# Optimization experiments

Hardware: AMD Instinct MI355X
Metric: run time of the kernel (lower is better)

The kernel has to match this reference:

```python
import jax, jax.numpy as jnp
import numpy as np

B, C, IN, H = 64, 128, 1024, 512  # batch, channels, input features (=='seq_length' arg), hidden


def setup_inputs() -> dict:
    key = jax.random.key(0)
    ks = jax.random.split(key, 9)
    s = 1.0 / np.sqrt(H)  # PyTorch LSTM init: U(-1/sqrt(H), 1/sqrt(H))
    u = lambda k, shape: jax.random.uniform(k, shape, jnp.float32, -s, s)
    return {
        "x": jax.random.normal(ks[0], (B, C, IN), jnp.float32),
        # layer 0: one weight set per direction (fwd, bwd)
        "W_ih0": u(ks[1], (2, 4 * H, IN)),
        "W_hh0": u(ks[2], (2, 4 * H, H)),
        "b_ih0": u(ks[3], (2, 4 * H)),
        "b_hh0": u(ks[4], (2, 4 * H)),
        # layers 1..2: input is concat of both directions (2H)
        "W_ih12": u(ks[5], (2, 2, 4 * H, 2 * H)),
        "W_hh12": u(ks[6], (2, 2, 4 * H, H)),
        "b_ih12": u(ks[7], (2, 2, 4 * H)),
        "b_hh12": u(ks[8], (2, 2, 4 * H)),
    }


def _cell(inp, W_ih, b_ih, b_hh):
    # One LSTM step from zero state (h0 = c0 = 0): W_hh @ h0 == 0, f*c0 == 0.
    gates = inp @ W_ih.T + b_ih + b_hh  # [N, 4H]
    i, f, g, o = jnp.split(gates, 4, axis=-1)  # PyTorch gate order: i, f, g, o
    c = jax.nn.sigmoid(i) * jnp.tanh(g)
    return jax.nn.sigmoid(o) * jnp.tanh(c)  # h, shape [N, H]


def reference(x, W_ih0, W_hh0, b_ih0, b_hh0, W_ih12, W_hh12, b_ih12, b_hh12):
    b, c, n = x.shape
    # Each channel is an independent seq-len-1 LSTM call with zero init state,
    # so fold channels into the batch dimension. W_hh* contribute nothing (h0=0).
    xb = x.reshape(b * c, n)
    h = jnp.concatenate(
        [_cell(xb, W_ih0[d], b_ih0[d], b_hh0[d]) for d in range(2)], axis=-1
    )  # [b*c, 2H]
    for l in range(2):  # layers 1 and 2
        h = jnp.concatenate(
            [_cell(h, W_ih12[l, d], b_ih12[l, d], b_hh12[l, d]) for d in range(2)],
            axis=-1,
        )
    return h.reshape(b, c, 2 * H)  # [batch, channels, 2*hidden]
```

## Files before the change

### kernel.cpp

```cpp
#include <hip/hip_runtime.h>


typedef float f32x4 __attribute__((ext_vector_type(4)));
typedef short short8 __attribute__((ext_vector_type(8)));
typedef unsigned short u16;

#define NP 3072
#define MROWS 8192
#define KDIM 1024
#define BM 256
#define BN 384
#define BK 32
#define LDS_TILE 40960

__device__ __forceinline__ u16 f2bf(float f) {
  unsigned u = __float_as_uint(f);
  u += 0x7fffu + ((u >> 16) & 1u);
  return (u16)(u >> 16);
}
__device__ __forceinline__ float sigmoid_f(float x) {
  return 1.0f / (1.0f + __expf(-x));
}
__device__ __forceinline__ float tanh_f(float x) {
  float xc = fminf(fmaxf(x, -15.0f), 15.0f);
  float e = __expf(2.0f * xc);
  return (e - 1.0f) / (e + 1.0f);
}
__device__ __forceinline__ void gload_lds16(const void* g, void* l) {
  __builtin_amdgcn_global_load_lds((const __attribute__((address_space(1))) void*)g,
                                   (__attribute__((address_space(3))) void*)l,
                                   16, 0, 0);
}


__global__ __launch_bounds__(256) void k_convert_x(const float* __restrict__ x,
                                                   u16* __restrict__ out) {
  int tid = blockIdx.x * 256 + threadIdx.x;
  const float4* src = (const float4*)x + (size_t)tid * 2;
  float4 v0 = src[0], v1 = src[1];
  union { u16 u[8]; uint4 v; } r;
  r.u[0] = f2bf(v0.x); r.u[1] = f2bf(v0.y); r.u[2] = f2bf(v0.z); r.u[3] = f2bf(v0.w);
  r.u[4] = f2bf(v1.x); r.u[5] = f2bf(v1.y); r.u[6] = f2bf(v1.z); r.u[7] = f2bf(v1.w);
  ((uint4*)out)[tid] = r.v;
}

__global__ __launch_bounds__(256) void k_pack_w(const float* __restrict__ Wih0,
                                                const float* __restrict__ Wih12,
                                                u16* __restrict__ P) {
  int tid = blockIdx.x * 256 + threadIdx.x;
  int s   = tid / (NP * 128);
  int rem = tid - s * (NP * 128);
  int p   = rem >> 7;
  int k8  = rem & 127;
  int hb = p / 48;
  int pr = p - hb * 48;
  int gs = pr >> 4;
  int hl = pr & 15;
  int hcol = hb * 16 + hl;
  int dir = hcol >> 9;
  int h   = hcol & 511;
  int og  = (gs == 0) ? 0 : (gs + 1);
  const float* src;
  if (s == 0)
    src = Wih0 + ((size_t)(dir * 2048 + og * 512 + h)) * 1024 + k8 * 8;
  else
    src = Wih12 + ((size_t)(((s - 1) * 2 + dir) * 2048 + og * 512 + h)) * 1024 + k8 * 8;
  float4 v0 = ((const float4*)src)[0];
  float4 v1 = ((const float4*)src)[1];
  union { u16 u[8]; uint4 v; } r;
  r.u[0] = f2bf(v0.x); r.u[1] = f2bf(v0.y); r.u[2] = f2bf(v0.z); r.u[3] = f2bf(v0.w);
  r.u[4] = f2bf(v1.x); r.u[5] = f2bf(v1.y); r.u[6] = f2bf(v1.z); r.u[7] = f2bf(v1.w);
  ((uint4*)P)[tid] = r.v;
}

__global__ __launch_bounds__(256) void k_pack_bias(const float* __restrict__ bih0,
                                                   const float* __restrict__ bhh0,
                                                   const float* __restrict__ bih12,
                                                   const float* __restrict__ bhh12,
                                                   float* __restrict__ pb) {
  int tid = blockIdx.x * 256 + threadIdx.x;
  if (tid >= 3 * NP) return;
  int s = tid / NP;
  int p = tid - s * NP;
  int hb = p / 48;
  int pr = p - hb * 48;
  int gs = pr >> 4;
  int hl = pr & 15;
  int hcol = hb * 16 + hl;
  int dir = hcol >> 9;
  int h   = hcol & 511;
  int og  = (gs == 0) ? 0 : (gs + 1);
  int j   = og * 512 + h;
  float v;
  if (s == 0) {
    int i = dir * 2048 + j;
    v = bih0[i] + bhh0[i];
  } else {
    int i = ((s - 1) * 2 + dir) * 2048 + j;
    v = bih12[i] + bhh12[i];
  }
  pb[tid] = v;
}


#define BAR()    __builtin_amdgcn_s_barrier()
#define SCHEDB() __builtin_amdgcn_sched_barrier(0)
#define WAITV(N) asm volatile("s_waitcnt vmcnt(" #N ")" ::: "memory")
#define MM(Macc, Aop, Bop) Macc = __builtin_amdgcn_mfma_f32_16x16x32_bf16(Aop, Bop, Macc, 0, 0, 0)

#define STAGE(BUF, KT) \
  { char* dst = lds + (BUF) * LDS_TILE + t * 16; \
    gload_lds16(srcA + (size_t)(KT) * BK,               dst); \
    gload_lds16(srcA + 128 * KDIM + (size_t)(KT) * BK,  dst + 8192); \
    gload_lds16(srcB + (size_t)(KT) * BK,               dst + 16384); \
    gload_lds16(srcB + 128 * KDIM + (size_t)(KT) * BK,  dst + 24576); \
    gload_lds16(srcB + 256 * KDIM + (size_t)(KT) * BK,  dst + 32768); }

#define KSTEP(RBUF, SBUF, KT, DOST, LASTT) \
  { \
    if (DOST) { STAGE(SBUF, (KT) + 2); } \
    const char* base = lds + (RBUF) * LDS_TILE; \
    short8 a0 = *(const short8*)(base + aBase); \
    short8 a1 = *(const short8*)(base + aBase + 1024); \
    short8 a2 = *(const short8*)(base + aBase + 2048); \
    short8 a3 = *(const short8*)(base + aBase + 3072); \
    short8 a4 = *(const short8*)(base + aBase + 4096); \
    short8 a5 = *(const short8*)(base + aBase + 5120); \
    short8 a6 = *(const short8*)(base + aBase + 6144); \
    short8 a7 = *(const short8*)(base + aBase + 7168); \
    short8 b0 = *(const short8*)(base + bBase); \
    short8 b1 = *(const short8*)(base + bBase + 1024); \
    short8 b2 = *(const short8*)(base + bBase + 2048); \
    __builtin_amdgcn_s_setprio(1); \
    MM(acc[0][0], a0, b0); MM(acc[1][0], a1, b0); MM(acc[2][0], a2, b0); MM(acc[3][0], a3, b0); \
    MM(acc[4][0], a4, b0); MM(acc[5][0], a5, b0); MM(acc[6][0], a6, b0); MM(acc[7][0], a7, b0); \
    MM(acc[0][1], a0, b1); MM(acc[1][1], a1, b1); MM(acc[2][1], a2, b1); MM(acc[3][1], a3, b1); \
    MM(acc[4][1], a4, b1); MM(acc[5][1], a5, b1); MM(acc[6][1], a6, b1); MM(acc[7][1], a7, b1); \
    MM(acc[0][2], a0, b2); MM(acc[1][2], a1, b2); MM(acc[2][2], a2, b2); MM(acc[3][2], a3, b2); \
    MM(acc[4][2], a4, b2); MM(acc[5][2], a5, b2); MM(acc[6][2], a6, b2); MM(acc[7][2], a7, b2); \
    __builtin_amdgcn_s_setprio(0); \
    b0 = *(const short8*)(base + bBase + 3072); \
    b1 = *(const short8*)(base + bBase + 4096); \
    b2 = *(const short8*)(base + bBase + 5120); \
    __builtin_amdgcn_s_setprio(1); \
    MM(acc[0][3], a0, b0); MM(acc[1][3], a1, b0); MM(acc[2][3], a2, b0); MM(acc[3][3], a3, b0); \
    MM(acc[4][3], a4, b0); MM(acc[5][3], a5, b0); MM(acc[6][3], a6, b0); MM(acc[7][3], a7, b0); \
    MM(acc[0][4], a0, b1); MM(acc[1][4], a1, b1); MM(acc[2][4], a2, b1); MM(acc[3][4], a3, b1); \
    MM(acc[4][4], a4, b1); MM(acc[5][4], a5, b1); MM(acc[6][4], a6, b1); MM(acc[7][4], a7, b1); \
    MM(acc[0][5], a0, b2); MM(acc[1][5], a1, b2); MM(acc[2][5], a2, b2); MM(acc[3][5], a3, b2); \
    MM(acc[4][5], a4, b2); MM(acc[5][5], a5, b2); MM(acc[6][5], a6, b2); MM(acc[7][5], a7, b2); \
    __builtin_amdgcn_s_setprio(0); \
    if (DOST) { WAITV(5); } \
    else if (!(LASTT)) { WAITV(0); } \
    if (!(LASTT)) { BAR(); SCHEDB(); } \
  }

template <bool F32OUT>
__global__ __launch_bounds__(512, 2) void k_lstm_gemmW(const u16* __restrict__ A,
                                                       const u16* __restrict__ Bp,
                                                       const float* __restrict__ bias,
                                                       void* __restrict__ outp) {
  __shared__ __align__(16) char lds[3 * LDS_TILE];
  const int t    = threadIdx.x;
  const int lane = t & 63;
  const int w    = t >> 6;
  const int wr   = w >> 2;
  const int wc   = w & 3;
  const int r16  = lane & 15, kg = lane >> 4;

  const int n_hw = blockIdx.y * gridDim.x + blockIdx.x;
  const int c    = n_hw & 7;
  const int wlc  = n_hw >> 3;
  const int bx   = (c & 1) * 4 + (wlc & 3);
  const int by   = (c >> 1) * 8 + (wlc >> 2);
  const int brow = by * BM;
  const int bn0  = bx * BN;

  const int slot = (kg ^ ((r16 >> 1) & 3)) << 4;
  const int aBase = wr * 8192 + r16 * 64 + slot;
  const int bBase = 16384 + wc * 6144 + r16 * 64 + slot;

  const int srow = t >> 2;
  const int koct = ((t & 3) ^ ((t >> 3) & 3)) << 3;
  const u16* srcA = A  + (size_t)(brow + srow) * KDIM + koct;
  const u16* srcB = Bp + (size_t)(bn0  + srow) * KDIM + koct;

  f32x4 acc[8][6];
#pragma unroll
  for (int m = 0; m < 8; ++m)
#pragma unroll
    for (int n = 0; n < 6; ++n) acc[m][n] = (f32x4){0.f, 0.f, 0.f, 0.f};

  STAGE(0, 0);
  STAGE(1, 1);
  WAITV(5);
  BAR(); SCHEDB();

  for (int k3 = 0; k3 < 10; ++k3) {
    int kt = k3 * 3;
    KSTEP(0, 2, kt + 0, 1, 0);
    KSTEP(1, 0, kt + 1, 1, 0);
    KSTEP(2, 1, kt + 2, 1, 0);
  }
  KSTEP(0, 0, 30, 0, 0);
  KSTEP(1, 0, 31, 0, 1);

#pragma unroll
  for (int trio = 0; trio < 2; ++trio) {
    int pbase = bn0 + wc * 96 + trio * 48;
    float biV = bias[pbase + r16];
    float bgV = bias[pbase + 16 + r16];
    float boV = bias[pbase + 32 + r16];
    int hcol = (bx * 8 + wc * 2 + trio) * 16 + r16;
#pragma unroll
    for (int m = 0; m < 8; ++m) {
      int rowb = brow + wr * 128 + m * 16 + kg * 4;
#pragma unroll
      for (int r = 0; r < 4; ++r) {
        float vi = acc[m][trio * 3 + 0][r] + biV;
        float vg = acc[m][trio * 3 + 1][r] + bgV;
        float vo = acc[m][trio * 3 + 2][r] + boV;
        float c2 = sigmoid_f(vi) * tanh_f(vg);
        float hv = sigmoid_f(vo) * tanh_f(c2);
        size_t oidx = (size_t)(rowb + r) * 1024 + hcol;
        if (F32OUT) ((float*)outp)[oidx] = hv;
        else        ((u16*)outp)[oidx]   = f2bf(hv);
      }
    }
  }
}

extern "C" void kernel_launch(void* const* d_in, const int* in_sizes, int n_in,
                              void* d_out, int out_size, void* d_ws, size_t ws_size,
                              hipStream_t stream) {
  const float* x     = (const float*)d_in[0];
  const float* Wih0  = (const float*)d_in[1];
  const float* bih0  = (const float*)d_in[3];
  const float* bhh0  = (const float*)d_in[4];
  const float* Wih12 = (const float*)d_in[5];
  const float* bih12 = (const float*)d_in[7];
  const float* bhh12 = (const float*)d_in[8];

  char* ws = (char*)d_ws;
  u16*   xbf = (u16*)ws;
  u16*   h1  = (u16*)(ws + 16777216);
  u16*   h2  = (u16*)(ws + 33554432);
  u16*   P3  = (u16*)(ws + 50331648);
  float* pb3 = (float*)(ws + 69206016);

  k_convert_x<<<4096, 256, 0, stream>>>(x, xbf);
  k_pack_w<<<4608, 256, 0, stream>>>(Wih0, Wih12, P3);
  k_pack_bias<<<36, 256, 0, stream>>>(bih0, bhh0, bih12, bhh12, pb3);

  dim3 grid(NP / BN, MROWS / BM);
  k_lstm_gemmW<false><<<grid, 512, 0, stream>>>(xbf, P3, pb3, h1);
  k_lstm_gemmW<false><<<grid, 512, 0, stream>>>(h1, P3 + (size_t)NP * KDIM, pb3 + NP, h2);
  k_lstm_gemmW<true ><<<grid, 512, 0, stream>>>(h2, P3 + (size_t)2 * NP * KDIM, pb3 + 2 * NP, d_out);
}
```

Measured before the change: 198.0 us.

## Halve GEMM tile width to 256x192 with 4 waves and double buffering

```diff
diff --git a/kernel.cpp b/kernel.cpp
--- a/kernel.cpp
+++ b/kernel.cpp
@@ -9,9 +9,9 @@
 #define MROWS 8192
 #define KDIM 1024
 #define BM 256
-#define BN 384
+#define BN 192
 #define BK 32
-#define LDS_TILE 40960
+#define LDS_TILE 28672
 
 __device__ __forceinline__ u16 f2bf(float f) {
   unsigned u = __float_as_uint(f);
@@ -111,68 +111,68 @@
 #define STAGE(BUF, KT) \
   { char* dst = lds + (BUF) * LDS_TILE + t * 16; \
     gload_lds16(srcA + (size_t)(KT) * BK,               dst); \
+    gload_lds16(srcA + 64 * KDIM + (size_t)(KT) * BK,   dst + 4096); \
     gload_lds16(srcA + 128 * KDIM + (size_t)(KT) * BK,  dst + 8192); \
+    gload_lds16(srcA + 192 * KDIM + (size_t)(KT) * BK,  dst + 12288); \
     gload_lds16(srcB + (size_t)(KT) * BK,               dst + 16384); \
-    gload_lds16(srcB + 128 * KDIM + (size_t)(KT) * BK,  dst + 24576); \
-    gload_lds16(srcB + 256 * KDIM + (size_t)(KT) * BK,  dst + 32768); }
-
-#define KSTEP(RBUF, SBUF, KT, DOST, LASTT) \
+    gload_lds16(srcB + 64 * KDIM + (size_t)(KT) * BK,   dst + 20480); \
+    gload_lds16(srcB + 128 * KDIM + (size_t)(KT) * BK,  dst + 24576); }
+
+#define KSTEP(RBUF, KT, DOST, LASTT) \
   { \
-    if (DOST) { STAGE(SBUF, (KT) + 2); } \
+    if (DOST) { STAGE((RBUF)^1, (KT)+1); } \
     const char* base = lds + (RBUF) * LDS_TILE; \
     short8 a0 = *(const short8*)(base + aBase); \
     short8 a1 = *(const short8*)(base + aBase + 1024); \
     short8 a2 = *(const short8*)(base + aBase + 2048); \
     short8 a3 = *(const short8*)(base + aBase + 3072); \
-    short8 a4 = *(const short8*)(base + aBase + 4096); \
-    short8 a5 = *(const short8*)(base + aBase + 5120); \
-    short8 a6 = *(const short8*)(base + aBase + 6144); \
-    short8 a7 = *(const short8*)(base + aBase + 7168); \
     short8 b0 = *(const short8*)(base + bBase); \
     short8 b1 = *(const short8*)(base + bBase + 1024); \
     short8 b2 = *(const short8*)(base + bBase + 2048); \
+    short8 b3 = *(const short8*)(base + bBase + 3072); \
+    short8 b4 = *(const short8*)(base + bBase + 4096); \
+    short8 b5 = *(const short8*)(base + bBase + 5120); \
     __builtin_amdgcn_s_setprio(1); \
     MM(acc[0][0], a0, b0); MM(acc[1][0], a1, b0); MM(acc[2][0], a2, b0); MM(acc[3][0], a3, b0); \
-    MM(acc[4][0], a4, b0); MM(acc[5][0], a5, b0); MM(acc[6][0], a6, b0); MM(acc[7][0], a7, b0); \
     MM(acc[0][1], a0, b1); MM(acc[1][1], a1, b1); MM(acc[2][1], a2, b1); MM(acc[3][1], a3, b1); \
-    MM(acc[4][1], a4, b1); MM(acc[5][1], a5, b1); MM(acc[6][1], a6, b1); MM(acc[7][1], a7, b1); \
     MM(acc[0][2], a0, b2); MM(acc[1][2], a1, b2); MM(acc[2][2], a2, b2); MM(acc[3][2], a3, b2); \
-    MM(acc[4][2], a4, b2); MM(acc[5][2], a5, b2); MM(acc[6][2], a6, b2); MM(acc[7][2], a7, b2); \
+    MM(acc[0][3], a0, b3); MM(acc[1][3], a1, b3); MM(acc[2][3], a2, b3); MM(acc[3][3], a3, b3); \
+    MM(acc[0][4], a0, b4); MM(acc[1][4], a1, b4); MM(acc[2][4], a2, b4); MM(acc[3][4], a3, b4); \
+    MM(acc[0][5], a0, b5); MM(acc[1][5], a1, b5); MM(acc[2][5], a2, b5); MM(acc[3][5], a3, b5); \
     __builtin_amdgcn_s_setprio(0); \
-    b0 = *(const short8*)(base + bBase + 3072); \
-    b1 = *(const short8*)(base + bBase + 4096); \
-    b2 = *(const short8*)(base + bBase + 5120); \
+    a0 = *(const short8*)(base + aBase + 4096); \
+    a1 = *(const short8*)(base + aBase + 5120); \
+    a2 = *(const short8*)(base + aBase + 6144); \
+    a3 = *(const short8*)(base + aBase + 7168); \
     __builtin_amdgcn_s_setprio(1); \
-    MM(acc[0][3], a0, b0); MM(acc[1][3], a1, b0); MM(acc[2][3], a2, b0); MM(acc[3][3], a3, b0); \
-    MM(acc[4][3], a4, b0); MM(acc[5][3], a5, b0); MM(acc[6][3], a6, b0); MM(acc[7][3], a7, b0); \
-    MM(acc[0][4], a0, b1); MM(acc[1][4], a1, b1); MM(acc[2][4], a2, b1); MM(acc[3][4], a3, b1); \
-    MM(acc[4][4], a4, b1); MM(acc[5][4], a5, b1); MM(acc[6][4], a6, b1); MM(acc[7][4], a7, b1); \
-    MM(acc[0][5], a0, b2); MM(acc[1][5], a1, b2); MM(acc[2][5], a2, b2); MM(acc[3][5], a3, b2); \
-    MM(acc[4][5], a4, b2); MM(acc[5][5], a5, b2); MM(acc[6][5], a6, b2); MM(acc[7][5], a7, b2); \
+    MM(acc[4][0], a0, b0); MM(acc[5][0], a1, b0); MM(acc[6][0], a2, b0); MM(acc[7][0], a3, b0); \
+    MM(acc[4][1], a0, b1); MM(acc[5][1], a1, b1); MM(acc[6][1], a2, b1); MM(acc[7][1], a3, b1); \
+    MM(acc[4][2], a0, b2); MM(acc[5][2], a1, b2); MM(acc[6][2], a2, b2); MM(acc[7][2], a3, b2); \
+    MM(acc[4][3], a0, b3); MM(acc[5][3], a1, b3); MM(acc[6][3], a2, b3); MM(acc[7][3], a3, b3); \
+    MM(acc[4][4], a0, b4); MM(acc[5][4], a1, b4); MM(acc[6][4], a2, b4); MM(acc[7][4], a3, b4); \
+    MM(acc[4][5], a0, b5); MM(acc[5][5], a1, b5); MM(acc[6][5], a2, b5); MM(acc[7][5], a3, b5); \
     __builtin_amdgcn_s_setprio(0); \
-    if (DOST) { WAITV(5); } \
-    else if (!(LASTT)) { WAITV(0); } \
-    if (!(LASTT)) { BAR(); SCHEDB(); } \
+    if (!(LASTT)) { WAITV(0); BAR(); SCHEDB(); } \
   }
 
 template <bool F32OUT>
-__global__ __launch_bounds__(512, 2) void k_lstm_gemmW(const u16* __restrict__ A,
-                                                       const u16* __restrict__ Bp,
-                                                       const float* __restrict__ bias,
-                                                       void* __restrict__ outp) {
-  __shared__ __align__(16) char lds[3 * LDS_TILE];
+__global__ __launch_bounds__(256) void k_lstm_gemm2b(const u16* __restrict__ A,
+                                                     const u16* __restrict__ Bp,
+                                                     const float* __restrict__ bias,
+                                                     void* __restrict__ outp) {
+  __shared__ __align__(16) char lds[2 * LDS_TILE];
   const int t    = threadIdx.x;
   const int lane = t & 63;
   const int w    = t >> 6;
-  const int wr   = w >> 2;
-  const int wc   = w & 3;
+  const int wr   = w >> 1;
+  const int wc   = w & 1;
   const int r16  = lane & 15, kg = lane >> 4;
 
   const int n_hw = blockIdx.y * gridDim.x + blockIdx.x;
   const int c    = n_hw & 7;
   const int wlc  = n_hw >> 3;
-  const int bx   = (c & 1) * 4 + (wlc & 3);
-  const int by   = (c >> 1) * 8 + (wlc >> 2);
+  const int bx   = (c & 1) * 8 + (wlc & 7);
+  const int by   = (c >> 1) * 8 + (wlc >> 3);
   const int brow = by * BM;
   const int bn0  = bx * BN;
 
@@ -192,18 +192,15 @@
     for (int n = 0; n < 6; ++n) acc[m][n] = (f32x4){0.f, 0.f, 0.f, 0.f};
 
   STAGE(0, 0);
-  STAGE(1, 1);
-  WAITV(5);
+  WAITV(0);
   BAR(); SCHEDB();
 
-  for (int k3 = 0; k3 < 10; ++k3) {
-    int kt = k3 * 3;
-    KSTEP(0, 2, kt + 0, 1, 0);
-    KSTEP(1, 0, kt + 1, 1, 0);
-    KSTEP(2, 1, kt + 2, 1, 0);
-  }
-  KSTEP(0, 0, 30, 0, 0);
-  KSTEP(1, 0, 31, 0, 1);
+  for (int k2 = 0; k2 < 15; ++k2) {
+    KSTEP(0, 2 * k2, 1, 0);
+    KSTEP(1, 2 * k2 + 1, 1, 0);
+  }
+  KSTEP(0, 30, 1, 0);
+  KSTEP(1, 31, 0, 1);
 
 #pragma unroll
   for (int trio = 0; trio < 2; ++trio) {
@@ -211,7 +208,7 @@
     float biV = bias[pbase + r16];
     float bgV = bias[pbase + 16 + r16];
     float boV = bias[pbase + 32 + r16];
-    int hcol = (bx * 8 + wc * 2 + trio) * 16 + r16;
+    int hcol = (bx * 4 + wc * 2 + trio) * 16 + r16;
 #pragma unroll
     for (int m = 0; m < 8; ++m) {
       int rowb = brow + wr * 128 + m * 16 + kg * 4;
@@ -253,7 +250,7 @@
   k_pack_bias<<<36, 256, 0, stream>>>(bih0, bhh0, bih12, bhh12, pb3);
 
   dim3 grid(NP / BN, MROWS / BM);
-  k_lstm_gemmW<false><<<grid, 512, 0, stream>>>(xbf, P3, pb3, h1);
-  k_lstm_gemmW<false><<<grid, 512, 0, stream>>>(h1, P3 + (size_t)NP * KDIM, pb3 + NP, h2);
-  k_lstm_gemmW<true ><<<grid, 512, 0, stream>>>(h2, P3 + (size_t)2 * NP * KDIM, pb3 + 2 * NP, d_out);
-}
+  k_lstm_gemm2b<false><<<grid, 256, 0, stream>>>(xbf, P3, pb3, h1);
+  k_lstm_gemm2b<false><<<grid, 256, 0, stream>>>(h1, P3 + (size_t)NP * KDIM, pb3 + NP, h2);
+  k_lstm_gemm2b<true ><<<grid, 256, 0, stream>>>(h2, P3 + (size_t)2 * NP * KDIM, pb3 + 2 * NP, d_out);
+}
```

New measurement: 228.4 us. 15.4% more time.
